# Optimization experiments

Measured on AMD Instinct MI355X. Metric: run time of the kernel, lower is better.

Reference implementation:

```python
import jax, jax.numpy as jnp
import numpy as np

# dims: B nodes, K hops, N neighbors/node, channels/features per FeatTrans1d stage
B, K, N = 512, 2, 32
C0, F0 = 1, 512
C1, F1 = 4, 16
C2, F2 = 32, 1
NUM_CLASS = 40
EPS_BN = 1e-5
EPS_NORM = 1e-7


def softsign(x):
    return x / (1.0 + jnp.abs(x))


def sgnroot(x):
    return jnp.sign(x) * jnp.sqrt(jnp.abs(x))


def row_normalize(x):
    # normalize over axis 1 as in the torch code; NaN -> 0
    x = x / (jnp.abs(x).sum(axis=1, keepdims=True) + EPS_NORM)
    return jnp.where(jnp.isnan(x), 0.0, x)


def feature_adjacency(x, nb):
    # x: [B,C,F], nb: [B,N,C,F] -> fadj: [B,F,F]
    fadj = jnp.einsum('bcf,bncg->bfg', x, nb)
    fadj = fadj + jnp.swapaxes(fadj, -1, -2)
    return row_normalize(sgnroot(fadj))


def transform(x, fadj, W):
    # x: [B,C,F], fadj: [B,F,G], W: [D,C,G,E] -> [B,D,E]
    xg = jnp.einsum('bcf,bfg->bcg', x, fadj)
    return jnp.einsum('bcg,dcge->bde', xg, W)


def transform_nb(nb, fadj, W):
    # nb: [B,N,C,F], fadj: [B,F,G] (node i's fadj broadcast over its N neighbors)
    xg = jnp.einsum('bncf,bfg->bncg', nb, fadj)
    return jnp.einsum('bncg,dcge->bnde', xg, W)


def bn(x, gamma, beta, axes, ch_axis):
    # training-mode BatchNorm1d: batch stats per channel (biased variance)
    mean = x.mean(axes, keepdims=True)
    var = x.var(axes, keepdims=True)
    shape = [1] * x.ndim
    shape[ch_axis] = x.shape[ch_axis]
    return (x - mean) * jax.lax.rsqrt(var + EPS_BN) * gamma.reshape(shape) + beta.reshape(shape)


def setup_inputs() -> dict:
    key = jax.random.key(0)
    ks = jax.random.split(key, 8)
    x = jax.random.normal(ks[0], (B, C0, F0), jnp.float32)
    neighbor = jax.random.normal(ks[1], (B, K, N, C0, F0), jnp.float32)
    W1 = jax.random.normal(ks[2], (K, C1, C0, F0, F1), jnp.float32) * 0.05
    W2 = jax.random.normal(ks[3], (K, C2, C1, F1, F2), jnp.float32) * 0.1
    g1 = jnp.ones((K, C1), jnp.float32)
    b1 = jnp.zeros((K, C1), jnp.float32)
    g2 = jnp.ones((K, C2), jnp.float32)
    b2 = jnp.zeros((K, C2), jnp.float32)
    Wc1 = jax.random.normal(ks[4], (C2 * F2 * K, C2 * F2), jnp.float32) * 0.1
    bc1 = jnp.zeros((C2 * F2,), jnp.float32)
    Wc2 = jax.random.normal(ks[5], (C2 * F2, NUM_CLASS), jnp.float32) * 0.1
    bc2 = jnp.zeros((NUM_CLASS,), jnp.float32)
    return {"x": x, "neighbor": neighbor, "W1": W1, "g1": g1, "b1": b1,
            "W2": W2, "g2": g2, "b2": b2,
            "Wc1": Wc1, "bc1": bc1, "Wc2": Wc2, "bc2": bc2}


def reference(x, neighbor, W1, g1, b1, W2, g2, b2, Wc1, bc1, Wc2, bc2):
    outs = []
    for kk in range(K):  # fixed small hop count, structurally distinct weights
        nb_k = neighbor[:, kk]                      # [B,N,C0,F0]
        fadj1 = feature_adjacency(x, nb_k)          # [B,F0,F0]
        h = transform(x, fadj1, W1[kk])             # [B,C1,F1]
        nbh = transform_nb(nb_k, fadj1, W1[kk])     # [B,N,C1,F1]
        # BN over batch+feature dims for h; per-node BN over (N,F) for neighbors
        h = softsign(bn(h, g1[kk], b1[kk], (0, 2), 1))
        nbh = softsign(bn(nbh, g1[kk], b1[kk], (1, 3), 2))
        fadj2 = feature_adjacency(h, nbh)           # [B,F1,F1]
        h2 = transform(h, fadj2, W2[kk])            # [B,C2,F2]
        h2 = softsign(bn(h2, g2[kk], b2[kk], (0, 2), 1))
        outs.append(h2)
    x_khops = jnp.concatenate(outs, axis=1)         # [B, C2*K, F2]
    flat = x_khops.reshape(B, -1)                   # dropout is identity at eval
    hid = jax.nn.relu(flat @ Wc1 + bc1)
    return hid @ Wc2 + bc2                          # [B, NUM_CLASS]
```

## Files before the change

### kernel.cpp

```cpp
#include <hip/hip_runtime.h>
#include <hip/hip_bf16.h>

#define B_SZ 512
#define KHOP 2
#define NNB  32
#define F0   512
#define C1   4
#define F1   16
#define C2   32
#define NCLS 40

#define EPS_BN   1e-5f
#define EPS_NORM 1e-7f

typedef __attribute__((ext_vector_type(8))) short short8;
typedef __attribute__((ext_vector_type(8))) unsigned short us8;
typedef __attribute__((ext_vector_type(4))) float f32x4;

__device__ __forceinline__ float softsignf(float v) { return v / (1.0f + fabsf(v)); }

__device__ __forceinline__ unsigned short f2bf(float f) {
    __hip_bfloat16 h = __float2bfloat16(f);
    unsigned short u;
    __builtin_memcpy(&u, &h, 2);
    return u;
}

__global__ __launch_bounds__(256) void k_prep(const float* __restrict__ W1,
                                              unsigned short* __restrict__ w1t)
{
    const int idx = blockIdx.x * 256 + threadIdx.x;
    const int g  = idx & 511;
    const int de = (idx >> 9) & 63;
    const int kk = idx >> 15;
    const int d = de >> 4, e = de & 15;
    w1t[idx] = f2bf(W1[((size_t)((kk * 4 + d) * 512) + g) * 16 + e]);
}

#define SMEM_MAIN 74752

__global__ __launch_bounds__(256, 2) void k_main(
    const float* __restrict__ xg_, const float* __restrict__ nbg,
    const float* __restrict__ W1, const unsigned short* __restrict__ w1t,
    const float* __restrict__ g1, const float* __restrict__ b1,
    float* __restrict__ h_raw, float* __restrict__ nbs_out)
{
    extern __shared__ char smem[];
    float* xl   = (float*)(smem + 65536);
    float* sl   = (float*)(smem + 67584);
    float* invD = (float*)(smem + 69632);
    float* xgx  = (float*)(smem + 71680);
    float* redh = (float*)(smem + 73728);

    const int t = threadIdx.x;
    const int pair = blockIdx.x;
    const int b = pair >> 1, k = pair & 1;
    const int l = t & 63, w = t >> 6;

    {
        const float* nbp = nbg + (size_t)pair * (NNB * F0);
        float s0 = 0.f, s1 = 0.f;
        #pragma unroll
        for (int n = 0; n < NNB; ++n) {
            float v0 = nbp[n * F0 + t];
            float v1 = nbp[n * F0 + t + 256];
            s0 += v0; s1 += v1;
            *(unsigned short*)(smem + n * 1024 + ((2 * t) ^ ((n & 7) << 4))) = f2bf(v0);
            *(unsigned short*)(smem + n * 1024 + ((2 * (t + 256)) ^ ((n & 7) << 4))) = f2bf(v1);
        }
        sl[t] = s0; sl[t + 256] = s1;
        xl[t] = xg_[b * F0 + t];
        xl[t + 256] = xg_[b * F0 + t + 256];
    }
    __syncthreads();

    const int gA = t, gB = t + 256;
    const float xa = xl[gA], xb = xl[gB];
    const float sa = sl[gA], sb = sl[gB];
    float accDa = 0.f, accXa = 0.f, accDb = 0.f, accXb = 0.f;

    f32x4 acc[2][8];
    #pragma unroll
    for (int m = 0; m < 2; ++m)
        #pragma unroll
        for (int j = 0; j < 8; ++j)
            acc[m][j] = (f32x4){0.f, 0.f, 0.f, 0.f};

    const int swA = ((gA >> 1) & 3) << 4;
    const int swB = ((gB >> 1) & 3) << 4;
    const int kol = l >> 4;

    #pragma unroll 1
    for (int strip = 0; strip < 16; ++strip) {
        const int f0 = strip * 32;
        #pragma unroll
        for (int ko = 0; ko < 4; ++ko) {
            float4 xf0 = ((const float4*)xl)[(f0 >> 2) + ko * 2];
            float4 xf1 = ((const float4*)xl)[(f0 >> 2) + ko * 2 + 1];
            float4 sf0 = ((const float4*)sl)[(f0 >> 2) + ko * 2];
            float4 sf1 = ((const float4*)sl)[(f0 >> 2) + ko * 2 + 1];
            const float xf[8] = {xf0.x, xf0.y, xf0.z, xf0.w, xf1.x, xf1.y, xf1.z, xf1.w};
            const float sf[8] = {sf0.x, sf0.y, sf0.z, sf0.w, sf1.x, sf1.y, sf1.z, sf1.w};
            us8 va, vb;
            #pragma unroll
            for (int i = 0; i < 8; ++i) {
                float r1 = xf[i] * sa + xa * sf[i];
                float a1 = sqrtf(fabsf(r1));
                accDa += a1;
                float v1 = copysignf(a1, r1);
                accXa += xf[i] * v1;
                va[i] = f2bf(v1);
                float r2 = xf[i] * sb + xb * sf[i];
                float a2 = sqrtf(fabsf(r2));
                accDb += a2;
                float v2 = copysignf(a2, r2);
                accXb += xf[i] * v2;
                vb[i] = f2bf(v2);
            }
            *(us8*)(smem + 32768 + gA * 64 + ((ko * 16) ^ swA)) = va;
            *(us8*)(smem + 32768 + gB * 64 + ((ko * 16) ^ swB)) = vb;
        }
        __syncthreads();
        short8 afrag[2];
        #pragma unroll
        for (int m = 0; m < 2; ++m) {
            const int n = m * 16 + (l & 15);
            afrag[m] = *(const short8*)(smem + n * 1024 +
                        ((f0 * 2 + kol * 16) ^ ((n & 7) << 4)));
        }
        #pragma unroll
        for (int j = 0; j < 8; ++j) {
            const int g = w * 128 + j * 16 + (l & 15);
            short8 bfrag = *(const short8*)(smem + 32768 + g * 64 +
                            ((kol * 16) ^ (((g >> 1) & 3) << 4)));
            acc[0][j] = __builtin_amdgcn_mfma_f32_16x16x32_bf16(afrag[0], bfrag, acc[0][j], 0, 0, 0);
            acc[1][j] = __builtin_amdgcn_mfma_f32_16x16x32_bf16(afrag[1], bfrag, acc[1][j], 0, 0, 0);
        }
        __syncthreads();
    }

    {
        const float ia = 1.f / (accDa + EPS_NORM);
        const float ib = 1.f / (accDb + EPS_NORM);
        invD[gA] = ia; xgx[gA] = accXa * ia;
        invD[gB] = ib; xgx[gB] = accXb * ib;
    }
    __syncthreads();

    #pragma unroll
    for (int m = 0; m < 2; ++m)
        #pragma unroll
        for (int j = 0; j < 8; ++j) {
            const int g = w * 128 + j * 16 + (l & 15);
            const float iv = invD[g];
            #pragma unroll
            for (int r = 0; r < 4; ++r) {
                const int n = m * 16 + (l >> 4) * 4 + r;
                *(unsigned short*)(smem + n * 1024 + ((2 * g) ^ ((n & 7) << 4))) =
                    f2bf(acc[m][j][r] * iv);
            }
        }
    __syncthreads();

    f32x4 acc3[2];
    acc3[0] = (f32x4){0.f, 0.f, 0.f, 0.f};
    acc3[1] = (f32x4){0.f, 0.f, 0.f, 0.f};
    {
        const int de = w * 16 + (l & 15);
        const unsigned short* wtp = w1t + ((size_t)(k * 64 + de) * 512) + kol * 8;
        #pragma unroll
        for (int ks = 0; ks < 16; ++ks) {
            short8 bfrag = *(const short8*)(wtp + ks * 32);
            #pragma unroll
            for (int m = 0; m < 2; ++m) {
                const int n = m * 16 + (l & 15);
                short8 af = *(const short8*)(smem + n * 1024 +
                            ((ks * 64 + kol * 16) ^ ((n & 7) << 4)));
                acc3[m] = __builtin_amdgcn_mfma_f32_16x16x32_bf16(af, bfrag, acc3[m], 0, 0, 0);
            }
        }
    }

    {
        float vals[8];
        float s1 = 0.f, s2 = 0.f;
        #pragma unroll
        for (int m = 0; m < 2; ++m)
            #pragma unroll
            for (int r = 0; r < 4; ++r) {
                float v = acc3[m][r];
                vals[m * 4 + r] = v; s1 += v; s2 += v * v;
            }
        #pragma unroll
        for (int off = 32; off >= 1; off >>= 1) {
            s1 += __shfl_xor(s1, off);
            s2 += __shfl_xor(s2, off);
        }
        const float mean = s1 * (1.f / 512.f);
        const float var  = s2 * (1.f / 512.f) - mean * mean;
        const float An   = g1[k * C1 + w] * rsqrtf(var + EPS_BN);
        const float Bn   = b1[k * C1 + w] - mean * An;
        float nbse = 0.f;
        #pragma unroll
        for (int i = 0; i < 8; ++i) nbse += softsignf(vals[i] * An + Bn);
        nbse += __shfl_xor(nbse, 16);
        nbse += __shfl_xor(nbse, 32);
        if (l < 16) nbs_out[pair * 64 + w * 16 + l] = nbse;
    }

    {
        const int de2 = t & 63, gs = t >> 6;
        const int d = de2 >> 4, e = de2 & 15;
        const float* Wp = W1 + ((size_t)(k * 4 + d) * 512) * 16 + e;
        float acch = 0.f;
        const int gbeg = gs * 128;
        #pragma unroll 8
        for (int gi = 0; gi < 128; ++gi)
            acch += xgx[gbeg + gi] * Wp[(gbeg + gi) * 16];
        redh[gs * 64 + de2] = acch;
    }
    __syncthreads();
    if (t < 64)
        h_raw[pair * 64 + t] = redh[t] + redh[64 + t] + redh[128 + t] + redh[192 + t];
}

__global__ __launch_bounds__(256) void k_hstats(
    const float* __restrict__ h_rawg, const float* __restrict__ g1,
    const float* __restrict__ b1, float* __restrict__ hstats)
{
    const int kd = blockIdx.x;
    const int k = kd >> 2, d = kd & 3;
    float s1 = 0.f, s2 = 0.f;
    for (int i = threadIdx.x; i < B_SZ * F1; i += 256) {
        const int bb = i >> 4, e = i & 15;
        float v = h_rawg[(bb * 2 + k) * 64 + d * 16 + e];
        s1 += v; s2 += v * v;
    }
    #pragma unroll
    for (int off = 32; off >= 1; off >>= 1) { s1 += __shfl_xor(s1, off); s2 += __shfl_xor(s2, off); }
    __shared__ float r1[4], r2[4];
    if ((threadIdx.x & 63) == 0) { r1[threadIdx.x >> 6] = s1; r2[threadIdx.x >> 6] = s2; }
    __syncthreads();
    if (threadIdx.x == 0) {
        float S1 = r1[0] + r1[1] + r1[2] + r1[3];
        float S2 = r2[0] + r2[1] + r2[2] + r2[3];
        float mean = S1 * (1.f / 8192.f);
        float var  = S2 * (1.f / 8192.f) - mean * mean;
        float A = g1[kd] * rsqrtf(var + EPS_BN);
        hstats[kd] = A;
        hstats[8 + kd] = b1[kd] - mean * A;
    }
}

__global__ __launch_bounds__(256) void k_stage2(
    const float* __restrict__ h_rawg, const float* __restrict__ nbsg,
    const float* __restrict__ hstats, const float* __restrict__ W2,
    float* __restrict__ h2_raw)
{
    __shared__ float hl[4][64], nl[4][64], fl[4][256], xg2l[4][64];
    const int t = threadIdx.x, wv = t >> 6, l = t & 63;
    const int pair = blockIdx.x * 4 + wv;
    const int k = pair & 1;
    const int d = l >> 4;
    float hv = h_rawg[pair * 64 + l];
    hl[wv][l] = softsignf(hv * hstats[k * 4 + d] + hstats[8 + k * 4 + d]);
    nl[wv][l] = nbsg[pair * 64 + l];
    __syncthreads();
    const int gcol = l & 15;
    float raw[4];
    #pragma unroll
    for (int j = 0; j < 4; ++j) {
        const int idx = l + 64 * j;
        const int f = idx >> 4;
        float a = 0.f;
        #pragma unroll
        for (int c = 0; c < 4; ++c) a += hl[wv][c * 16 + f] * nl[wv][c * 16 + gcol];
        raw[j] = a;
        fl[wv][idx] = a;
    }
    __syncthreads();
    float w4[4]; float Dp = 0.f;
    #pragma unroll
    for (int j = 0; j < 4; ++j) {
        const int idx = l + 64 * j;
        const int f = idx >> 4;
        float v = raw[j] + fl[wv][gcol * 16 + f];
        float a = sqrtf(fabsf(v));
        Dp += a;
        w4[j] = copysignf(a, v);
    }
    Dp += __shfl_xor(Dp, 16);
    Dp += __shfl_xor(Dp, 32);
    const float invD = 1.f / (Dp + EPS_NORM);
    __syncthreads();
    #pragma unroll
    for (int j = 0; j < 4; ++j) fl[wv][l + 64 * j] = w4[j] * invD;
    __syncthreads();
    {
        const int c = l >> 4;
        float a = 0.f;
        #pragma unroll
        for (int f = 0; f < 16; ++f) a += hl[wv][c * 16 + f] * fl[wv][f * 16 + gcol];
        xg2l[wv][c * 16 + gcol] = a;
    }
    __syncthreads();
    if (l < 32) {
        const float* W2p = W2 + k * (C2 * C1 * F1) + l * (C1 * F1);
        float a = 0.f;
        #pragma unroll
        for (int i = 0; i < 64; ++i) a += xg2l[wv][i] * W2p[i];
        h2_raw[pair * 32 + l] = a;
    }
}

__global__ __launch_bounds__(256) void k_h2stats(
    const float* __restrict__ h2_raw, const float* __restrict__ g2,
    const float* __restrict__ b2, float* __restrict__ h2st)
{
    const int kd = blockIdx.x;
    const int k = kd >> 5, d = kd & 31;
    float s1 = 0.f, s2 = 0.f;
    for (int bb = threadIdx.x; bb < B_SZ; bb += 256) {
        float v = h2_raw[(bb * 2 + k) * 32 + d];
        s1 += v; s2 += v * v;
    }
    #pragma unroll
    for (int off = 32; off >= 1; off >>= 1) { s1 += __shfl_xor(s1, off); s2 += __shfl_xor(s2, off); }
    __shared__ float r1[4], r2[4];
    if ((threadIdx.x & 63) == 0) { r1[threadIdx.x >> 6] = s1; r2[threadIdx.x >> 6] = s2; }
    __syncthreads();
    if (threadIdx.x == 0) {
        float S1 = r1[0] + r1[1] + r1[2] + r1[3];
        float S2 = r2[0] + r2[1] + r2[2] + r2[3];
        float mean = S1 * (1.f / 512.f);
        float var  = S2 * (1.f / 512.f) - mean * mean;
        float A = g2[kd] * rsqrtf(var + EPS_BN);
        h2st[kd] = A;
        h2st[64 + kd] = b2[kd] - mean * A;
    }
}

__global__ __launch_bounds__(64) void k_cls(
    const float* __restrict__ h2_raw, const float* __restrict__ h2st,
    const float* __restrict__ Wc1, const float* __restrict__ bc1,
    const float* __restrict__ Wc2, const float* __restrict__ bc2,
    float* __restrict__ out)
{
    __shared__ float flat[64];
    __shared__ float hid[32];
    const int b = blockIdx.x, l = threadIdx.x;
    const int k = l >> 5, d = l & 31;
    float v = h2_raw[(b * 2 + k) * 32 + d];
    flat[l] = softsignf(v * h2st[l] + h2st[64 + l]);
    __syncthreads();
    if (l < 32) {
        float a = bc1[l];
        #pragma unroll
        for (int i = 0; i < 64; ++i) a += flat[i] * Wc1[i * 32 + l];
        hid[l] = fmaxf(a, 0.f);
    }
    __syncthreads();
    if (l < NCLS) {
        float a = bc2[l];
        #pragma unroll
        for (int j = 0; j < 32; ++j) a += hid[j] * Wc2[j * NCLS + l];
        out[b * NCLS + l] = a;
    }
}

extern "C" void kernel_launch(void* const* d_in, const int* in_sizes, int n_in,
                              void* d_out, int out_size, void* d_ws, size_t ws_size,
                              hipStream_t stream)
{
    const float* x   = (const float*)d_in[0];
    const float* nbg = (const float*)d_in[1];
    const float* W1  = (const float*)d_in[2];
    const float* g1  = (const float*)d_in[3];
    const float* b1  = (const float*)d_in[4];
    const float* W2  = (const float*)d_in[5];
    const float* g2  = (const float*)d_in[6];
    const float* b2  = (const float*)d_in[7];
    const float* Wc1 = (const float*)d_in[8];
    const float* bc1 = (const float*)d_in[9];
    const float* Wc2 = (const float*)d_in[10];
    const float* bc2 = (const float*)d_in[11];
    float* out = (float*)d_out;
    float* ws  = (float*)d_ws;

    float* h_raw  = ws;
    float* nbs    = ws + 65536;
    float* hstats = ws + 131072;
    float* h2_raw = ws + 131136;
    float* h2st   = ws + 163904;
    unsigned short* w1t = (unsigned short*)h2_raw;

    hipLaunchKernelGGL(k_prep,    dim3(256),            dim3(256), 0, stream, W1, w1t);
    hipLaunchKernelGGL(k_main,    dim3(B_SZ * KHOP),    dim3(256), SMEM_MAIN, stream,
                       x, nbg, W1, w1t, g1, b1, h_raw, nbs);
    hipLaunchKernelGGL(k_hstats,  dim3(KHOP * C1),      dim3(256), 0, stream,
                       h_raw, g1, b1, hstats);
    hipLaunchKernelGGL(k_stage2,  dim3(B_SZ * KHOP / 4), dim3(256), 0, stream,
                       h_raw, nbs, hstats, W2, h2_raw);
    hipLaunchKernelGGL(k_h2stats, dim3(KHOP * C2),      dim3(256), 0, stream,
                       h2_raw, g2, b2, h2st);
    hipLaunchKernelGGL(k_cls,     dim3(B_SZ),           dim3(64), 0, stream,
                       h2_raw, h2st, Wc1, bc1, Wc2, bc2, out);
}
```

Baseline: 310.7 us.

## Fuse BN stat kernels via atomics, drop weight prep, vectorize neighbor loads

Removes the k_prep, k_hstats and k_h2stats launches. Batch-norm sums are now accumulated with atomicAdd from k_main and k_stage2 into a buffer zeroed by a memset, and each consumer finalises mean and variance itself. W1 is read strided and converted to bf16 inside k_main instead of being pre-transposed. Neighbor loading switches to float4 reads with packed bf16 conversion, the neighbor sums are reduced through shared memory, and the accumulators are split in two to shorten dependency chains. In exchange it adds atomic contention, strided uncoalesced W1 reads, and reduction order that is no longer deterministic.

```diff
diff --git a/kernel.cpp b/kernel.cpp
--- a/kernel.cpp
+++ b/kernel.cpp
@@ -14,36 +14,24 @@
 #define EPS_NORM 1e-7f
 
 typedef __attribute__((ext_vector_type(8))) short short8;
-typedef __attribute__((ext_vector_type(8))) unsigned short us8;
 typedef __attribute__((ext_vector_type(4))) float f32x4;
 
 __device__ __forceinline__ float softsignf(float v) { return v / (1.0f + fabsf(v)); }
 
-__device__ __forceinline__ unsigned short f2bf(float f) {
-    __hip_bfloat16 h = __float2bfloat16(f);
-    unsigned short u;
-    __builtin_memcpy(&u, &h, 2);
-    return u;
-}
-
-__global__ __launch_bounds__(256) void k_prep(const float* __restrict__ W1,
-                                              unsigned short* __restrict__ w1t)
-{
-    const int idx = blockIdx.x * 256 + threadIdx.x;
-    const int g  = idx & 511;
-    const int de = (idx >> 9) & 63;
-    const int kk = idx >> 15;
-    const int d = de >> 4, e = de & 15;
-    w1t[idx] = f2bf(W1[((size_t)((kk * 4 + d) * 512) + g) * 16 + e]);
+__device__ __forceinline__ unsigned cvt_pk_bf16(float lo, float hi) {
+    unsigned r;
+    asm("v_cvt_pk_bf16_f32 %0, %1, %2" : "=v"(r) : "v"(lo), "v"(hi));
+    return r;
 }
 
 #define SMEM_MAIN 74752
 
 __global__ __launch_bounds__(256, 2) void k_main(
     const float* __restrict__ xg_, const float* __restrict__ nbg,
-    const float* __restrict__ W1, const unsigned short* __restrict__ w1t,
+    const float* __restrict__ W1,
     const float* __restrict__ g1, const float* __restrict__ b1,
-    float* __restrict__ h_raw, float* __restrict__ nbs_out)
+    float* __restrict__ h_raw, float* __restrict__ nbs_out,
+    float* __restrict__ hsum)
 {
     extern __shared__ char smem[];
     float* xl   = (float*)(smem + 65536);
@@ -58,26 +46,45 @@
     const int l = t & 63, w = t >> 6;
 
     {
+        const int oct = t & 63, ng = t >> 6;
+        const int f0s = oct * 8;
         const float* nbp = nbg + (size_t)pair * (NNB * F0);
-        float s0 = 0.f, s1 = 0.f;
-        #pragma unroll
-        for (int n = 0; n < NNB; ++n) {
-            float v0 = nbp[n * F0 + t];
-            float v1 = nbp[n * F0 + t + 256];
-            s0 += v0; s1 += v1;
-            *(unsigned short*)(smem + n * 1024 + ((2 * t) ^ ((n & 7) << 4))) = f2bf(v0);
-            *(unsigned short*)(smem + n * 1024 + ((2 * (t + 256)) ^ ((n & 7) << 4))) = f2bf(v1);
-        }
-        sl[t] = s0; sl[t + 256] = s1;
-        xl[t] = xg_[b * F0 + t];
+        float sp0=0,sp1=0,sp2=0,sp3=0,sp4=0,sp5=0,sp6=0,sp7=0;
+        #pragma unroll
+        for (int ni = 0; ni < 8; ++ni) {
+            const int n = ng * 8 + ni;
+            float4 q0 = *(const float4*)(nbp + n * F0 + f0s);
+            float4 q1 = *(const float4*)(nbp + n * F0 + f0s + 4);
+            sp0 += q0.x; sp1 += q0.y; sp2 += q0.z; sp3 += q0.w;
+            sp4 += q1.x; sp5 += q1.y; sp6 += q1.z; sp7 += q1.w;
+            uint4 p;
+            p.x = cvt_pk_bf16(q0.x, q0.y);
+            p.y = cvt_pk_bf16(q0.z, q0.w);
+            p.z = cvt_pk_bf16(q1.x, q1.y);
+            p.w = cvt_pk_bf16(q1.z, q1.w);
+            *(uint4*)(smem + n * 1024 + ((2 * f0s) ^ ((n & 7) << 4))) = p;
+        }
+        float* part = (float*)(smem + 32768);
+        *(float4*)(part + ng * 512 + f0s)     = make_float4(sp0, sp1, sp2, sp3);
+        *(float4*)(part + ng * 512 + f0s + 4) = make_float4(sp4, sp5, sp6, sp7);
+        xl[t]       = xg_[b * F0 + t];
         xl[t + 256] = xg_[b * F0 + t + 256];
+    }
+    __syncthreads();
+    {
+        const float* part = (const float*)(smem + 32768);
+        float sA = part[t] + part[512 + t] + part[1024 + t] + part[1536 + t];
+        float sB = part[t + 256] + part[512 + t + 256]
+                 + part[1024 + t + 256] + part[1536 + t + 256];
+        sl[t] = sA; sl[t + 256] = sB;
     }
     __syncthreads();
 
     const int gA = t, gB = t + 256;
     const float xa = xl[gA], xb = xl[gB];
     const float sa = sl[gA], sb = sl[gB];
-    float accDa = 0.f, accXa = 0.f, accDb = 0.f, accXb = 0.f;
+    float dA0=0.f, dA1=0.f, dB0=0.f, dB1=0.f;
+    float xA0=0.f, xA1=0.f, xB0=0.f, xB1=0.f;
 
     f32x4 acc[2][8];
     #pragma unroll
@@ -101,24 +108,29 @@
             float4 sf1 = ((const float4*)sl)[(f0 >> 2) + ko * 2 + 1];
             const float xf[8] = {xf0.x, xf0.y, xf0.z, xf0.w, xf1.x, xf1.y, xf1.z, xf1.w};
             const float sf[8] = {sf0.x, sf0.y, sf0.z, sf0.w, sf1.x, sf1.y, sf1.z, sf1.w};
-            us8 va, vb;
+            uint pa[4], pb[4];
+            float vpA = 0.f, vpB = 0.f;
             #pragma unroll
             for (int i = 0; i < 8; ++i) {
-                float r1 = xf[i] * sa + xa * sf[i];
-                float a1 = sqrtf(fabsf(r1));
-                accDa += a1;
-                float v1 = copysignf(a1, r1);
-                accXa += xf[i] * v1;
-                va[i] = f2bf(v1);
-                float r2 = xf[i] * sb + xb * sf[i];
-                float a2 = sqrtf(fabsf(r2));
-                accDb += a2;
-                float v2 = copysignf(a2, r2);
-                accXb += xf[i] * v2;
-                vb[i] = f2bf(v2);
+                float rA = xf[i] * sa + xa * sf[i];
+                float aA = sqrtf(fabsf(rA));
+                float vA = copysignf(aA, rA);
+                float rB = xf[i] * sb + xb * sf[i];
+                float aB = sqrtf(fabsf(rB));
+                float vB = copysignf(aB, rB);
+                if (i & 1) {
+                    dA1 += aA; dB1 += aB; xA1 += xf[i] * vA; xB1 += xf[i] * vB;
+                    pa[i >> 1] = cvt_pk_bf16(vpA, vA);
+                    pb[i >> 1] = cvt_pk_bf16(vpB, vB);
+                } else {
+                    dA0 += aA; dB0 += aB; xA0 += xf[i] * vA; xB0 += xf[i] * vB;
+                    vpA = vA; vpB = vB;
+                }
             }
-            *(us8*)(smem + 32768 + gA * 64 + ((ko * 16) ^ swA)) = va;
-            *(us8*)(smem + 32768 + gB * 64 + ((ko * 16) ^ swB)) = vb;
+            uint4 ua; ua.x = pa[0]; ua.y = pa[1]; ua.z = pa[2]; ua.w = pa[3];
+            uint4 ub; ub.x = pb[0]; ub.y = pb[1]; ub.z = pb[2]; ub.w = pb[3];
+            *(uint4*)(smem + 32768 + gA * 64 + ((ko * 16) ^ swA)) = ua;
+            *(uint4*)(smem + 32768 + gB * 64 + ((ko * 16) ^ swB)) = ub;
         }
         __syncthreads();
         short8 afrag[2];
@@ -140,10 +152,10 @@
     }
 
     {
-        const float ia = 1.f / (accDa + EPS_NORM);
-        const float ib = 1.f / (accDb + EPS_NORM);
-        invD[gA] = ia; xgx[gA] = accXa * ia;
-        invD[gB] = ib; xgx[gB] = accXb * ib;
+        const float ia = 1.f / ((dA0 + dA1) + EPS_NORM);
+        const float ib = 1.f / ((dB0 + dB1) + EPS_NORM);
+        invD[gA] = ia; xgx[gA] = (xA0 + xA1) * ia;
+        invD[gB] = ib; xgx[gB] = (xB0 + xB1) * ib;
     }
     __syncthreads();
 
@@ -156,8 +168,9 @@
             #pragma unroll
             for (int r = 0; r < 4; ++r) {
                 const int n = m * 16 + (l >> 4) * 4 + r;
+                unsigned pv = cvt_pk_bf16(acc[m][j][r] * iv, 0.f);
                 *(unsigned short*)(smem + n * 1024 + ((2 * g) ^ ((n & 7) << 4))) =
-                    f2bf(acc[m][j][r] * iv);
+                    (unsigned short)pv;
             }
         }
     __syncthreads();
@@ -167,10 +180,20 @@
     acc3[1] = (f32x4){0.f, 0.f, 0.f, 0.f};
     {
         const int de = w * 16 + (l & 15);
-        const unsigned short* wtp = w1t + ((size_t)(k * 64 + de) * 512) + kol * 8;
-        #pragma unroll
+        const int d3 = de >> 4, e3 = de & 15;
+        const float* Wp3 = W1 + ((k * 4 + d3) * 512) * 16 + e3;
+        #pragma unroll 2
         for (int ks = 0; ks < 16; ++ks) {
-            short8 bfrag = *(const short8*)(wtp + ks * 32);
+            const int gg0 = ks * 32 + kol * 8;
+            float w0 = Wp3[(gg0 + 0) * 16], w1 = Wp3[(gg0 + 1) * 16];
+            float w2 = Wp3[(gg0 + 2) * 16], w3 = Wp3[(gg0 + 3) * 16];
+            float w4 = Wp3[(gg0 + 4) * 16], w5 = Wp3[(gg0 + 5) * 16];
+            float w6 = Wp3[(gg0 + 6) * 16], w7 = Wp3[(gg0 + 7) * 16];
+            uint4 bp;
+            bp.x = cvt_pk_bf16(w0, w1); bp.y = cvt_pk_bf16(w2, w3);
+            bp.z = cvt_pk_bf16(w4, w5); bp.w = cvt_pk_bf16(w6, w7);
+            short8 bfrag;
+            __builtin_memcpy(&bfrag, &bp, 16);
             #pragma unroll
             for (int m = 0; m < 2; ++m) {
                 const int n = m * 16 + (l & 15);
@@ -211,60 +234,55 @@
     {
         const int de2 = t & 63, gs = t >> 6;
         const int d = de2 >> 4, e = de2 & 15;
-        const float* Wp = W1 + ((size_t)(k * 4 + d) * 512) * 16 + e;
-        float acch = 0.f;
+        const float* Wp = W1 + ((k * 4 + d) * 512) * 16 + e;
+        float a0 = 0.f, a1 = 0.f;
         const int gbeg = gs * 128;
         #pragma unroll 8
-        for (int gi = 0; gi < 128; ++gi)
-            acch += xgx[gbeg + gi] * Wp[(gbeg + gi) * 16];
-        redh[gs * 64 + de2] = acch;
-    }
-    __syncthreads();
-    if (t < 64)
-        h_raw[pair * 64 + t] = redh[t] + redh[64 + t] + redh[128 + t] + redh[192 + t];
-}
-
-__global__ __launch_bounds__(256) void k_hstats(
-    const float* __restrict__ h_rawg, const float* __restrict__ g1,
-    const float* __restrict__ b1, float* __restrict__ hstats)
-{
-    const int kd = blockIdx.x;
-    const int k = kd >> 2, d = kd & 3;
-    float s1 = 0.f, s2 = 0.f;
-    for (int i = threadIdx.x; i < B_SZ * F1; i += 256) {
-        const int bb = i >> 4, e = i & 15;
-        float v = h_rawg[(bb * 2 + k) * 64 + d * 16 + e];
-        s1 += v; s2 += v * v;
-    }
-    #pragma unroll
-    for (int off = 32; off >= 1; off >>= 1) { s1 += __shfl_xor(s1, off); s2 += __shfl_xor(s2, off); }
-    __shared__ float r1[4], r2[4];
-    if ((threadIdx.x & 63) == 0) { r1[threadIdx.x >> 6] = s1; r2[threadIdx.x >> 6] = s2; }
-    __syncthreads();
-    if (threadIdx.x == 0) {
-        float S1 = r1[0] + r1[1] + r1[2] + r1[3];
-        float S2 = r2[0] + r2[1] + r2[2] + r2[3];
-        float mean = S1 * (1.f / 8192.f);
-        float var  = S2 * (1.f / 8192.f) - mean * mean;
-        float A = g1[kd] * rsqrtf(var + EPS_BN);
-        hstats[kd] = A;
-        hstats[8 + kd] = b1[kd] - mean * A;
+        for (int gi = 0; gi < 128; gi += 2) {
+            a0 += xgx[gbeg + gi]     * Wp[(gbeg + gi) * 16];
+            a1 += xgx[gbeg + gi + 1] * Wp[(gbeg + gi + 1) * 16];
+        }
+        redh[gs * 64 + de2] = a0 + a1;
+    }
+    __syncthreads();
+    if (t < 64) {
+        float hv = redh[t] + redh[64 + t] + redh[128 + t] + redh[192 + t];
+        h_raw[pair * 64 + t] = hv;
+        float s1 = hv, s2 = hv * hv;
+        #pragma unroll
+        for (int off = 1; off <= 8; off <<= 1) {
+            s1 += __shfl_xor(s1, off);
+            s2 += __shfl_xor(s2, off);
+        }
+        if ((t & 15) == 0) {
+            atomicAdd(&hsum[k * 4 + (t >> 4)], s1);
+            atomicAdd(&hsum[8 + k * 4 + (t >> 4)], s2);
+        }
     }
 }
 
 __global__ __launch_bounds__(256) void k_stage2(
     const float* __restrict__ h_rawg, const float* __restrict__ nbsg,
-    const float* __restrict__ hstats, const float* __restrict__ W2,
-    float* __restrict__ h2_raw)
+    const float* __restrict__ hsum,
+    const float* __restrict__ g1, const float* __restrict__ b1,
+    const float* __restrict__ W2,
+    float* __restrict__ h2_raw, float* __restrict__ h2sum)
 {
     __shared__ float hl[4][64], nl[4][64], fl[4][256], xg2l[4][64];
     const int t = threadIdx.x, wv = t >> 6, l = t & 63;
     const int pair = blockIdx.x * 4 + wv;
     const int k = pair & 1;
     const int d = l >> 4;
-    float hv = h_rawg[pair * 64 + l];
-    hl[wv][l] = softsignf(hv * hstats[k * 4 + d] + hstats[8 + k * 4 + d]);
-    nl[wv][l] = nbsg[pair * 64 + l];
+    {
+        const float S1 = hsum[k * 4 + d], S2 = hsum[8 + k * 4 + d];
+        const float mean = S1 * (1.f / 8192.f);
+        const float var  = S2 * (1.f / 8192.f) - mean * mean;
+        const float A = g1[k * 4 + d] * rsqrtf(var + EPS_BN);
+        const float Bc = b1[k * 4 + d] - mean * A;
+        float hv = h_rawg[pair * 64 + l];
+        hl[wv][l] = softsignf(hv * A + Bc);
+        nl[wv][l] = nbsg[pair * 64 + l];
+    }
     __syncthreads();
     const int gcol = l & 15;
     float raw[4];
@@ -310,38 +328,14 @@
         #pragma unroll
         for (int i = 0; i < 64; ++i) a += xg2l[wv][i] * W2p[i];
         h2_raw[pair * 32 + l] = a;
+        atomicAdd(&h2sum[k * 32 + l], a);
+        atomicAdd(&h2sum[64 + k * 32 + l], a * a);
     }
 }
 
-__global__ __launch_bounds__(256) void k_h2stats(
-    const float* __restrict__ h2_raw, const float* __restrict__ g2,
-    const float* __restrict__ b2, float* __restrict__ h2st)
-{
-    const int kd = blockIdx.x;
-    const int k = kd >> 5, d = kd & 31;
-    float s1 = 0.f, s2 = 0.f;
-    for (int bb = threadIdx.x; bb < B_SZ; bb += 256) {
-        float v = h2_raw[(bb * 2 + k) * 32 + d];
-        s1 += v; s2 += v * v;
-    }
-    #pragma unroll
-    for (int off = 32; off >= 1; off >>= 1) { s1 += __shfl_xor(s1, off); s2 += __shfl_xor(s2, off); }
-    __shared__ float r1[4], r2[4];
-    if ((threadIdx.x & 63) == 0) { r1[threadIdx.x >> 6] = s1; r2[threadIdx.x >> 6] = s2; }
-    __syncthreads();
-    if (threadIdx.x == 0) {
-        float S1 = r1[0] + r1[1] + r1[2] + r1[3];
-        float S2 = r2[0] + r2[1] + r2[2] + r2[3];
-        float mean = S1 * (1.f / 512.f);
-        float var  = S2 * (1.f / 512.f) - mean * mean;
-        float A = g2[kd] * rsqrtf(var + EPS_BN);
-        h2st[kd] = A;
-        h2st[64 + kd] = b2[kd] - mean * A;
-    }
-}
-
 __global__ __launch_bounds__(64) void k_cls(
-    const float* __restrict__ h2_raw, const float* __restrict__ h2st,
+    const float* __restrict__ h2_raw, const float* __restrict__ h2sum,
+    const float* __restrict__ g2, const float* __restrict__ b2,
     const float* __restrict__ Wc1, const float* __restrict__ bc1,
     const float* __restrict__ Wc2, const float* __restrict__ bc2,
     float* __restrict__ out)
@@ -350,8 +344,15 @@
     __shared__ float hid[32];
     const int b = blockIdx.x, l = threadIdx.x;
     const int k = l >> 5, d = l & 31;
-    float v = h2_raw[(b * 2 + k) * 32 + d];
-    flat[l] = softsignf(v * h2st[l] + h2st[64 + l]);
+    {
+        const float S1 = h2sum[l], S2 = h2sum[64 + l];
+        const float mean = S1 * (1.f / 512.f);
+        const float var  = S2 * (1.f / 512.f) - mean * mean;
+        const float A = g2[l] * rsqrtf(var + EPS_BN);
+        const float Bc = b2[l] - mean * A;
+        float v = h2_raw[(b * 2 + k) * 32 + d];
+        flat[l] = softsignf(v * A + Bc);
+    }
     __syncthreads();
     if (l < 32) {
         float a = bc1[l];
@@ -389,20 +390,16 @@
 
     float* h_raw  = ws;
     float* nbs    = ws + 65536;
-    float* hstats = ws + 131072;
-    float* h2_raw = ws + 131136;
-    float* h2st   = ws + 163904;
-    unsigned short* w1t = (unsigned short*)h2_raw;
-
-    hipLaunchKernelGGL(k_prep,    dim3(256),            dim3(256), 0, stream, W1, w1t);
-    hipLaunchKernelGGL(k_main,    dim3(B_SZ * KHOP),    dim3(256), SMEM_MAIN, stream,
-                       x, nbg, W1, w1t, g1, b1, h_raw, nbs);
-    hipLaunchKernelGGL(k_hstats,  dim3(KHOP * C1),      dim3(256), 0, stream,
-                       h_raw, g1, b1, hstats);
-    hipLaunchKernelGGL(k_stage2,  dim3(B_SZ * KHOP / 4), dim3(256), 0, stream,
-                       h_raw, nbs, hstats, W2, h2_raw);
-    hipLaunchKernelGGL(k_h2stats, dim3(KHOP * C2),      dim3(256), 0, stream,
-                       h2_raw, g2, b2, h2st);
-    hipLaunchKernelGGL(k_cls,     dim3(B_SZ),           dim3(64), 0, stream,
-                       h2_raw, h2st, Wc1, bc1, Wc2, bc2, out);
+    float* h2_raw = ws + 131072;
+    float* stats  = ws + 163840;
+    float* hsum   = stats;
+    float* h2sum  = stats + 16;
+
+    hipMemsetAsync(stats, 0, 144 * sizeof(float), stream);
+    hipLaunchKernelGGL(k_main,   dim3(B_SZ * KHOP),     dim3(256), SMEM_MAIN, stream,
+                       x, nbg, W1, g1, b1, h_raw, nbs, hsum);
+    hipLaunchKernelGGL(k_stage2, dim3(B_SZ * KHOP / 4), dim3(256), 0, stream,
+                       h_raw, nbs, hsum, g1, b1, W2, h2_raw, h2sum);
+    hipLaunchKernelGGL(k_cls,    dim3(B_SZ),            dim3(64), 0, stream,
+                       h2_raw, h2sum, g2, b2, Wc1, bc1, Wc2, bc2, out);
 }
```

Result: no change. 305.6 us (-1.6%).
